# Kernel tuning notes

Hardware: AMD Instinct MI355X
Metric: run time of the kernel (lower is better)

The kernel has to match this reference:

```python
import jax, jax.numpy as jnp
import numpy as np

NOPE, ROPE, VDIM, QKD = 128, 64, 128, 192
H = 16
EPS = 1e-6
SCALING = QKD ** -0.5


def rms_norm(x, w):
    xf = x.astype(jnp.float32)
    var = jnp.mean(xf * xf, axis=-1, keepdims=True)
    return (w * (xf * jax.lax.rsqrt(var + EPS))).astype(x.dtype)


def rotate_half(x):
    d = x.shape[-1] // 2
    return jnp.concatenate((-x[..., d:], x[..., :d]), axis=-1)


def apply_rope(q, k, cos, sin):
    # cos/sin: [B,S,D] -> unsqueeze head dim
    cos = cos[:, None, :, :]
    sin = sin[:, None, :, :]
    return q * cos + rotate_half(q) * sin, k * cos + rotate_half(k) * sin


def setup_inputs() -> dict:
    key = jax.random.key(0)
    ks = jax.random.split(key, 8)
    B, S, D = 2, 2048, 2048
    pos = jnp.arange(S, dtype=jnp.float32)
    inv_freq = 1.0 / (10000.0 ** (jnp.arange(0, ROPE, 2, dtype=jnp.float32) / ROPE))
    ang = pos[:, None] * inv_freq[None, :]            # [S, ROPE/2]
    emb = jnp.concatenate([ang, ang], axis=-1)        # [S, ROPE]
    cos = jnp.broadcast_to(jnp.cos(emb)[None], (B, S, ROPE))
    sin = jnp.broadcast_to(jnp.sin(emb)[None], (B, S, ROPE))
    s = lambda k, shp, fan: jax.random.normal(k, shp, jnp.float32) * (fan ** -0.5)
    return {
        "hidden_states": jax.random.normal(ks[0], (B, S, D), jnp.float32),
        "cos": cos,
        "sin": sin,
        "q_a_W": s(ks[1], (1536, D), D),
        "q_a_norm_w": jnp.ones((1536,), jnp.float32),
        "q_b_W": s(ks[2], (H * QKD, 1536), 1536),
        "kv_a_W": s(ks[3], (512 + ROPE, D), D),
        "kv_a_norm_w": jnp.ones((512,), jnp.float32),
        "kv_b_W": s(ks[4], (H * (NOPE + VDIM), 512), 512),
        "o_W": s(ks[5], (D, H * VDIM), H * VDIM),
    }


def reference(hidden_states, cos, sin, q_a_W, q_a_norm_w, q_b_W, kv_a_W,
              kv_a_norm_w, kv_b_W, o_W):
    B, S, D = hidden_states.shape
    # low-rank Q path
    q = rms_norm(hidden_states @ q_a_W.T, q_a_norm_w) @ q_b_W.T   # [B,S,H*QKD]
    q = q.reshape(B, S, H, QKD).transpose(0, 2, 1, 3)             # [B,H,S,QKD]
    q_pass, q_rot = q[..., :NOPE], q[..., NOPE:]
    # compressed KV path
    ckv = hidden_states @ kv_a_W.T                                # [B,S,512+ROPE]
    k_lat, k_rot = ckv[..., :512], ckv[..., 512:]
    kv = rms_norm(k_lat, kv_a_norm_w) @ kv_b_W.T                  # [B,S,H*(NOPE+VDIM)]
    kv = kv.reshape(B, S, H, NOPE + VDIM).transpose(0, 2, 1, 3)   # [B,H,S,*]
    k_pass, v = kv[..., :NOPE], kv[..., NOPE:]
    k_rot = k_rot.reshape(B, 1, S, ROPE)
    q_rot, k_rot = apply_rope(q_rot, k_rot, cos, sin)
    k_rot = jnp.broadcast_to(k_rot, (B, H, S, ROPE))
    query = jnp.concatenate((q_pass, q_rot), axis=-1)             # [B,H,S,QKD]
    key = jnp.concatenate((k_pass, k_rot), axis=-1)
    # eager causal attention
    scores = jnp.einsum('bhsd,bhtd->bhst', query, key) * SCALING
    causal = jnp.tril(jnp.ones((S, S), bool))
    scores = jnp.where(causal, scores, jnp.finfo(scores.dtype).min)
    attn = jax.nn.softmax(scores.astype(jnp.float32), axis=-1).astype(query.dtype)
    out = jnp.einsum('bhst,bhtd->bhsd', attn, v)                  # [B,H,S,VDIM]
    out = out.transpose(0, 2, 1, 3).reshape(B, S, H * VDIM)
    return out @ o_W.T
```

## Files before the change

### kernel.cpp

```cpp
#include <hip/hip_runtime.h>
#include <hip/hip_bf16.h>


typedef __bf16 bf16x8 __attribute__((ext_vector_type(8)));
typedef float floatx4 __attribute__((ext_vector_type(4)));
#define BF16 __hip_bfloat16

static __device__ __forceinline__ BF16 f2b(float x) { return __float2bfloat16(x); }
static __device__ __forceinline__ unsigned short b2u(BF16 x) { return *(unsigned short*)&x; }
static __device__ __forceinline__ float fast_exp2(float x) { return __builtin_amdgcn_exp2f(x); }

template<int CTRL>
static __device__ __forceinline__ float dpp_mov(float x) {
  int xi = __builtin_bit_cast(int, x);
  int yi = __builtin_amdgcn_update_dpp(xi, xi, CTRL, 0xF, 0xF, false);
  return __builtin_bit_cast(float, yi);
}
static __device__ __forceinline__ float row_allmax(float x) {
  x = fmaxf(x, dpp_mov<0xB1>(x));
  x = fmaxf(x, dpp_mov<0x4E>(x));
  x = fmaxf(x, dpp_mov<0x141>(x));
  x = fmaxf(x, dpp_mov<0x140>(x));
  return x;
}
static __device__ __forceinline__ float row_allsum(float x) {
  x += dpp_mov<0xB1>(x);
  x += dpp_mov<0x4E>(x);
  x += dpp_mov<0x141>(x);
  x += dpp_mov<0x140>(x);
  return x;
}

static __device__ __forceinline__ void load_lds16(const BF16* g, BF16* l) {
  __builtin_amdgcn_global_load_lds((__attribute__((address_space(1))) void*)(void*)g,
                                   (__attribute__((address_space(3))) void*)(void*)l,
                                   16, 0, 0);
}

struct CastArgs {
  const float* src[6];
  BF16* dst[6];
  long n[6];
};
__global__ void cast_multi_k(CastArgs a) {
  int r = blockIdx.y;
  long n = a.n[r];
  const float* __restrict__ x = a.src[r];
  BF16* __restrict__ y = a.dst[r];
  for (long i = ((long)blockIdx.x * 256 + threadIdx.x) * 4; i + 3 < n;
       i += (long)gridDim.x * 1024) {
    float4 v = *(const float4*)(x + i);
    y[i+0] = f2b(v.x); y[i+1] = f2b(v.y); y[i+2] = f2b(v.z); y[i+3] = f2b(v.w);
  }
}

template<int OUT_MODE>
static __device__ __forceinline__ void gemm_body(
    const BF16* __restrict__ A, const BF16* __restrict__ B, void* __restrict__ C,
    int M, int N, int K, const float* __restrict__ cosb, const float* __restrict__ sinb,
    BF16* __restrict__ P1, BF16* __restrict__ P2, int bx, int by, BF16* As, BF16* Bs) {
  int tid = threadIdx.x, wave = tid >> 6, lane = tid & 63;
  int wr = wave >> 1, wc = wave & 1, lr = lane & 15, quad = lane >> 4;
  long m0 = (long)by * 256, n0 = (long)bx * 128;

  long asrc[4]; int adst[4];
#pragma unroll
  for (int i = 0; i < 4; i++) {
    int c = wave*64 + lane + 512*i;
    int r = c >> 3, k = c & 7;
    asrc[i] = (m0 + r) * (long)K + ((k ^ (r & 7)) << 3);
    adst[i] = wave*512 + i*4096;
  }
  long bsrc[2]; int bdst[2];
#pragma unroll
  for (int i = 0; i < 2; i++) {
    int c = wave*64 + lane + 512*i;
    int r = c >> 3, k = c & 7;
    long bn = n0 + r; if (bn >= N) bn = N - 1;
    bsrc[i] = bn * (long)K + ((k ^ (r & 7)) << 3);
    bdst[i] = wave*512 + i*4096;
  }

  auto stage = [&](int bi, int kt) {
    long k0 = (long)kt << 6;
    BF16* Ad = As + bi*16384;
    BF16* Bd = Bs + bi*8192;
#pragma unroll
    for (int i = 0; i < 4; i++) load_lds16(A + asrc[i] + k0, Ad + adst[i]);
#pragma unroll
    for (int i = 0; i < 2; i++) load_lds16(B + bsrc[i] + k0, Bd + bdst[i]);
  };

  int aoff[4], boff[4];
#pragma unroll
  for (int i = 0; i < 4; i++) aoff[i] = (wr*64 + i*16 + lr) * 64;
#pragma unroll
  for (int j = 0; j < 4; j++) boff[j] = (wc*64 + j*16 + lr) * 64;
  int x0 = ((quad    ) ^ (lr & 7)) << 3;
  int x1 = ((quad ^ 4) ^ (lr & 7)) << 3;

  floatx4 acc[4][4] = {};
  int NT = K >> 6;

  stage(0, 0);
  stage(1, 1);
  asm volatile("s_waitcnt vmcnt(6)" ::: "memory");
  __builtin_amdgcn_s_barrier();

  int cur = 0;
  for (int t = 0; t < NT; t++) {
    const BF16* Ab = As + cur*16384;
    const BF16* Bb = Bs + cur*8192;
    bf16x8 a0[4], a1[4], b0[4], b1[4];
#pragma unroll
    for (int i = 0; i < 4; i++) {
      a0[i] = *(const bf16x8*)(Ab + aoff[i] + x0);
      a1[i] = *(const bf16x8*)(Ab + aoff[i] + x1);
    }
#pragma unroll
    for (int j = 0; j < 4; j++) {
      b0[j] = *(const bf16x8*)(Bb + boff[j] + x0);
      b1[j] = *(const bf16x8*)(Bb + boff[j] + x1);
    }
    asm volatile("s_waitcnt lgkmcnt(0)" ::: "memory");
    __builtin_amdgcn_s_barrier();
    if (t + 2 < NT) stage(cur, t + 2);
    __builtin_amdgcn_s_setprio(1);
#pragma unroll
    for (int i = 0; i < 4; i++)
#pragma unroll
      for (int j = 0; j < 4; j++)
        acc[i][j] = __builtin_amdgcn_mfma_f32_16x16x32_bf16(a0[i], b0[j], acc[i][j], 0, 0, 0);
#pragma unroll
    for (int i = 0; i < 4; i++)
#pragma unroll
      for (int j = 0; j < 4; j++)
        acc[i][j] = __builtin_amdgcn_mfma_f32_16x16x32_bf16(a1[i], b1[j], acc[i][j], 0, 0, 0);
    __builtin_amdgcn_s_setprio(0);
    if (t + 2 < NT)      { asm volatile("s_waitcnt vmcnt(6)" ::: "memory"); }
    else if (t + 1 < NT) { asm volatile("s_waitcnt vmcnt(0)" ::: "memory"); }
    __builtin_amdgcn_s_barrier();
    __builtin_amdgcn_sched_barrier(0);
    cur ^= 1;
  }

  long n0w = n0 + wc*64;
  const float SCALE_L2E = 0.104117546f;
#pragma unroll
  for (int i = 0; i < 4; i++) {
    long tok = m0 + wr*64 + i*16 + quad*4;
    long bb = tok >> 11, s = tok & 2047;
    if (OUT_MODE == 0) {
#pragma unroll
      for (int r = 0; r < 4; r++) {
        long row = tok + r;
#pragma unroll
        for (int j = 0; j < 4; j++) {
          long col = n0w + j*16 + lr;
          if (col < N) ((float*)C)[row*(long)N + col] = acc[i][j][r];
        }
      }
    } else if (OUT_MODE == 2) {
#pragma unroll
      for (int j = 0; j < 4; j++) {
        long col = n0w + j*16 + lr;
        long h = col >> 8, d = col & 255;
        if (d < 128) {
#pragma unroll
          for (int r = 0; r < 4; r++)
            P1[((bb*16 + h)*2048 + s + r)*192 + d] = f2b(acc[i][j][r]);
        } else {
          ushort4 pk;
          pk.x = b2u(f2b(acc[i][j][0])); pk.y = b2u(f2b(acc[i][j][1]));
          pk.z = b2u(f2b(acc[i][j][2])); pk.w = b2u(f2b(acc[i][j][3]));
          *(ushort4*)(P2 + ((bb*16 + h)*128 + d - 128)*2048 + s) = pk;
        }
      }
    } else {
      bool rope = ((n0w % 192) == 128);
#pragma unroll
      for (int r = 0; r < 4; r++) {
        long row = tok + r;
#pragma unroll
        for (int j = 0; j < 4; j++) {
          long col = n0w + j*16 + lr;
          float x = acc[i][j][r], val;
          if (rope) {
            int id = j*16 + lr;
            float partner = acc[i][j^2][r];
            float rot = (j < 2) ? -partner : partner;
            val = x*cosb[row*64 + id] + rot*sinb[row*64 + id];
          } else {
            val = x;
          }
          long h = col / 192, d = col % 192;
          P1[((bb*16 + h)*2048 + s + r)*192 + d] = f2b(val * SCALE_L2E);
        }
      }
    }
  }
}

__global__ __launch_bounds__(512) void gemm0_k(const BF16* __restrict__ A, const BF16* __restrict__ B,
                                               float* __restrict__ C, int M, int N, int K) {
  __shared__ __align__(16) BF16 As[2*256*64];
  __shared__ __align__(16) BF16 Bs[2*128*64];
  gemm_body<0>(A, B, C, M, N, K, nullptr, nullptr, nullptr, nullptr,
               blockIdx.x, blockIdx.y, As, Bs);
}

__global__ __launch_bounds__(512) void gemm_qkv_k(const BF16* __restrict__ qan, const BF16* __restrict__ Wqb,
                                                  const BF16* __restrict__ kvn, const BF16* __restrict__ Wkvb,
                                                  const float* __restrict__ cosb, const float* __restrict__ sinb,
                                                  BF16* __restrict__ Qt, BF16* __restrict__ Kt,
                                                  BF16* __restrict__ Vt) {
  __shared__ __align__(16) BF16 As[2*256*64];
  __shared__ __align__(16) BF16 Bs[2*128*64];
  int bid = blockIdx.x;
  if (bid < 384) {
    gemm_body<3>(qan, Wqb, nullptr, 4096, 3072, 1536, cosb, sinb, Qt, nullptr,
                 bid % 24, bid / 24, As, Bs);
  } else {
    bid -= 384;
    gemm_body<2>(kvn, Wkvb, nullptr, 4096, 4096, 512, nullptr, nullptr, Kt, Vt,
                 bid % 32, bid / 32, As, Bs);
  }
}

__global__ __launch_bounds__(256) void norms_k(const float* __restrict__ qakv,
                                               const float* __restrict__ qw, const float* __restrict__ kw,
                                               const float* __restrict__ cosb, const float* __restrict__ sinb,
                                               BF16* __restrict__ qan, BF16* __restrict__ kvn,
                                               BF16* __restrict__ Kt) {
  long row = blockIdx.x;
  const float* xr = qakv + row * 2112;
  int tid = threadIdx.x;
  __shared__ float red[4];
  {
    float ss = 0.f;
    for (int i = tid*4; i < 1536; i += 1024) {
      float4 v = *(const float4*)(xr + i);
      ss += v.x*v.x + v.y*v.y + v.z*v.z + v.w*v.w;
    }
#pragma unroll
    for (int off = 32; off > 0; off >>= 1) ss += __shfl_down(ss, off);
    if ((tid & 63) == 0) red[tid >> 6] = ss;
    __syncthreads();
    float rs = rsqrtf((red[0]+red[1]+red[2]+red[3]) / 1536.f + 1e-6f);
    BF16* yr = qan + row * 1536;
    for (int i = tid*4; i < 1536; i += 1024) {
      float4 v = *(const float4*)(xr + i);
      yr[i+0] = f2b(v.x * qw[i+0] * rs);
      yr[i+1] = f2b(v.y * qw[i+1] * rs);
      yr[i+2] = f2b(v.z * qw[i+2] * rs);
      yr[i+3] = f2b(v.w * qw[i+3] * rs);
    }
  }
  __syncthreads();
  {
    float ss = 0.f;
    for (int i = tid*4; i < 512; i += 1024) {
      float4 v = *(const float4*)(xr + 1536 + i);
      ss += v.x*v.x + v.y*v.y + v.z*v.z + v.w*v.w;
    }
#pragma unroll
    for (int off = 32; off > 0; off >>= 1) ss += __shfl_down(ss, off);
    if ((tid & 63) == 0) red[tid >> 6] = ss;
    __syncthreads();
    float rs = rsqrtf((red[0]+red[1]+red[2]+red[3]) / 512.f + 1e-6f);
    BF16* yr = kvn + row * 512;
    for (int i = tid*4; i < 512; i += 1024) {
      float4 v = *(const float4*)(xr + 1536 + i);
      yr[i+0] = f2b(v.x * kw[i+0] * rs);
      yr[i+1] = f2b(v.y * kw[i+1] * rs);
      yr[i+2] = f2b(v.z * kw[i+2] * rs);
      yr[i+3] = f2b(v.w * kw[i+3] * rs);
    }
  }
  if (tid < 64) {
    int i = tid;
    const float* kr = xr + 2048;
    float x = kr[i];
    float rot = (i < 32) ? -kr[i + 32] : kr[i - 32];
    BF16 v = f2b(x * cosb[row*64 + i] + rot * sinb[row*64 + i]);
    long b = row >> 11, s = row & 2047;
    long base = ((b*16)*2048 + s)*192 + 128 + i;
#pragma unroll
    for (int h = 0; h < 16; h++) Kt[base + (long)h*2048*192] = v;
  }
}

#define LK 200
#define LV 72
#define LP 72
__global__ __launch_bounds__(512) void flash_k(const BF16* __restrict__ Qt, const BF16* __restrict__ Kt,
                                               const BF16* __restrict__ Vt, BF16* __restrict__ O) {
  __shared__ __align__(16) BF16 Ks[64*LK];
  __shared__ __align__(16) BF16 Vs[128*LV];
  __shared__ __align__(16) BF16 Ps[8][16*LP];
  int tid = threadIdx.x, wave = tid >> 6, lane = tid & 63;
  int lr = lane & 15, quad = lane >> 4;
  int F = blockIdx.x;
  int g = F & 31, u = F >> 5;
  int qt = (u < 8) ? u : 23 - u;
  int h = g & 15, b = g >> 4;
  const BF16* Qb = Qt + ((long)(b*16 + h) * 2048) * 192;
  const BF16* Kb = Kt + ((long)(b*16 + h) * 2048) * 192;
  const BF16* Vb = Vt + ((long)(b*16 + h) * 128) * 2048;
  const float NEG_INF = -__builtin_inff();

  int krow[3], kcol[3];
#pragma unroll
  for (int i = 0; i < 3; i++) {
    int c = tid + 512*i;
    krow[i] = c / 24; kcol[i] = (c % 24) * 8;
  }
  int vrow[2], vcol[2];
#pragma unroll
  for (int i = 0; i < 2; i++) {
    int c = tid + 512*i;
    vrow[i] = c >> 3; vcol[i] = (c & 7) * 8;
  }

  bf16x8 kreg[3], vreg[2];
  auto stage_load = [&](int k0) {
#pragma unroll
    for (int i = 0; i < 3; i++)
      kreg[i] = *(const bf16x8*)(Kb + (long)(k0 + krow[i])*192 + kcol[i]);
#pragma unroll
    for (int i = 0; i < 2; i++)
      vreg[i] = *(const bf16x8*)(Vb + (long)vrow[i]*2048 + k0 + vcol[i]);
  };
  auto stage_store = [&]() {
#pragma unroll
    for (int i = 0; i < 3; i++)
      *(bf16x8*)(Ks + krow[i]*LK + kcol[i]) = kreg[i];
#pragma unroll
    for (int i = 0; i < 2; i++)
      *(bf16x8*)(Vs + vrow[i]*LV + vcol[i]) = vreg[i];
  };

  {
    int q0 = qt * 128;
    int wq0 = q0 + wave*16;
    bf16x8 qf[6];
    {
      const BF16* qp = Qb + (long)(wq0 + lr) * 192 + quad*8;
#pragma unroll
      for (int f = 0; f < 6; f++) qf[f] = *(const bf16x8*)(qp + f*32);
    }
    float m_i[4], l_i[4];
#pragma unroll
    for (int r = 0; r < 4; r++) { m_i[r] = NEG_INF; l_i[r] = 0.f; }
    floatx4 o_acc[8] = {};
    int nk = 2*qt + 2;
    stage_load(0);
    for (int kt = 0; kt < nk; kt++) {
      __syncthreads();
      stage_store();
      __syncthreads();
      if (kt + 1 < nk) stage_load((kt + 1) * 64);
      if (kt*64 > wq0 + 15) continue;
      floatx4 st[4];
      __builtin_amdgcn_s_setprio(1);
#pragma unroll
      for (int t = 0; t < 4; t++) {
        floatx4 c = {};
#pragma unroll
        for (int f = 0; f < 6; f++) {
          bf16x8 kf = *(const bf16x8*)(Ks + (t*16+lr)*LK + f*32 + quad*8);
          c = __builtin_amdgcn_mfma_f32_16x16x32_bf16(qf[f], kf, c, 0, 0, 0);
        }
        st[t] = c;
      }
      __builtin_amdgcn_s_setprio(0);
      float mt[4];
#pragma unroll
      for (int r = 0; r < 4; r++) mt[r] = NEG_INF;
      if (kt*64 + 63 > wq0) {
        int rbase = wq0 + quad*4 - kt*64;
#pragma unroll
        for (int t = 0; t < 4; t++) {
          int coff = t*16 + lr;
#pragma unroll
          for (int r = 0; r < 4; r++) {
            float sc = st[t][r];
            if (coff > rbase + r) sc = NEG_INF;
            st[t][r] = sc;
            mt[r] = fmaxf(mt[r], sc);
          }
        }
      } else {
#pragma unroll
        for (int t = 0; t < 4; t++)
#pragma unroll
          for (int r = 0; r < 4; r++) mt[r] = fmaxf(mt[r], st[t][r]);
      }
#pragma unroll
      for (int r = 0; r < 4; r++) mt[r] = row_allmax(mt[r]);
      float alpha[4], rsum[4];
#pragma unroll
      for (int r = 0; r < 4; r++) {
        float mn = fmaxf(m_i[r], mt[r]);
        alpha[r] = fast_exp2(m_i[r] - mn);
        m_i[r] = mn;
        rsum[r] = 0.f;
      }
#pragma unroll
      for (int t = 0; t < 4; t++)
#pragma unroll
        for (int r = 0; r < 4; r++) {
          float p = fast_exp2(st[t][r] - m_i[r]);
          st[t][r] = p;
          rsum[r] += p;
        }
#pragma unroll
      for (int r = 0; r < 4; r++) rsum[r] = row_allsum(rsum[r]);
#pragma unroll
      for (int r = 0; r < 4; r++) l_i[r] = l_i[r]*alpha[r] + rsum[r];
#pragma unroll
      for (int v = 0; v < 8; v++)
#pragma unroll
        for (int r = 0; r < 4; r++) o_acc[v][r] *= alpha[r];
#pragma unroll
      for (int t = 0; t < 4; t++)
#pragma unroll
        for (int r = 0; r < 4; r++)
          Ps[wave][(quad*4 + r)*LP + t*16 + lr] = f2b(st[t][r]);
      __builtin_amdgcn_s_setprio(1);
#pragma unroll
      for (int kc = 0; kc < 2; kc++) {
        bf16x8 pa = *(const bf16x8*)(&Ps[wave][lr*LP + kc*32 + quad*8]);
#pragma unroll
        for (int v = 0; v < 8; v++) {
          bf16x8 vf = *(const bf16x8*)(&Vs[(v*16+lr)*LV + kc*32 + quad*8]);
          o_acc[v] = __builtin_amdgcn_mfma_f32_16x16x32_bf16(pa, vf, o_acc[v], 0, 0, 0);
        }
      }
      __builtin_amdgcn_s_setprio(0);
    }
    long rowb = wq0 + quad*4;
#pragma unroll
    for (int v = 0; v < 8; v++)
#pragma unroll
      for (int r = 0; r < 4; r++) {
        long row = rowb + r;
        O[((long)b*2048 + row)*2048 + h*128 + v*16 + lr] = f2b(o_acc[v][r] / l_i[r]);
      }
  }
}

extern "C" void kernel_launch(void* const* d_in, const int* in_sizes, int n_in,
                              void* d_out, int out_size, void* d_ws, size_t ws_size,
                              hipStream_t stream) {
  const float* hidden      = (const float*)d_in[0];
  const float* cosb        = (const float*)d_in[1];
  const float* sinb        = (const float*)d_in[2];
  const float* q_a_W       = (const float*)d_in[3];
  const float* q_a_norm_w  = (const float*)d_in[4];
  const float* q_b_W       = (const float*)d_in[5];
  const float* kv_a_W      = (const float*)d_in[6];
  const float* kv_a_norm_w = (const float*)d_in[7];
  const float* kv_b_W      = (const float*)d_in[8];
  const float* o_W         = (const float*)d_in[9];
  float* out = (float*)d_out;

  const int Mrows = 4096;

  char* ws = (char*)d_ws; size_t off = 0;
  auto alloc = [&](size_t bytes) -> void* {
    void* p = ws + off; off = (off + bytes + 255) & ~(size_t)255; return p;
  };
  BF16* hb    = (BF16*)alloc((size_t)4096*2048*2);
  BF16* Wqakv = (BF16*)alloc((size_t)2112*2048*2);
  BF16* Wqb   = (BF16*)alloc((size_t)3072*1536*2);
  BF16* Wkvb  = (BF16*)alloc((size_t)4096*512*2);
  BF16* Wo    = (BF16*)alloc((size_t)2048*2048*2);
  float* qakv = (float*)alloc((size_t)4096*2112*4);
  BF16* qan   = (BF16*)alloc((size_t)4096*1536*2);
  BF16* kvn   = (BF16*)alloc((size_t)4096*512*2);
  BF16* Qt    = (BF16*)alloc((size_t)2*16*2048*192*2);
  BF16* Kt    = (BF16*)alloc((size_t)2*16*2048*192*2);
  BF16* Vt    = (BF16*)alloc((size_t)2*16*128*2048*2);
  BF16* attn  = (BF16*)alloc((size_t)4096*2048*2);

  CastArgs ca;
  ca.src[0] = hidden;  ca.dst[0] = hb;                 ca.n[0] = (long)4096*2048;
  ca.src[1] = q_a_W;   ca.dst[1] = Wqakv;              ca.n[1] = (long)1536*2048;
  ca.src[2] = kv_a_W;  ca.dst[2] = Wqakv + (long)1536*2048; ca.n[2] = (long)576*2048;
  ca.src[3] = q_b_W;   ca.dst[3] = Wqb;                ca.n[3] = (long)3072*1536;
  ca.src[4] = kv_b_W;  ca.dst[4] = Wkvb;               ca.n[4] = (long)4096*512;
  ca.src[5] = o_W;     ca.dst[5] = Wo;                 ca.n[5] = (long)2048*2048;
  cast_multi_k<<<dim3(1024, 6), dim3(256), 0, stream>>>(ca);

  gemm0_k<<<dim3(17, 16), dim3(512), 0, stream>>>(hb, Wqakv, qakv, Mrows, 2112, 2048);

  norms_k<<<dim3(4096), dim3(256), 0, stream>>>(qakv, q_a_norm_w, kv_a_norm_w,
                                                cosb, sinb, qan, kvn, Kt);

  gemm_qkv_k<<<dim3(896), dim3(512), 0, stream>>>(qan, Wqb, kvn, Wkvb, cosb, sinb, Qt, Kt, Vt);

  flash_k<<<dim3(512), dim3(512), 0, stream>>>(Qt, Kt, Vt, attn);

  gemm0_k<<<dim3(16, 16), dim3(512), 0, stream>>>(attn, Wo, out, Mrows, 2048, 2048);
}
```

Baseline: 446.3 us.

## Double-buffer K/V tiles in flash attention and add lazy softmax rescaling

K and V shared-memory tiles are double-buffered so the next tile is written into the alternate buffer after compute. This removes one of the two block-wide barriers per iteration and overlaps global loads with compute. Online-softmax rescaling of the accumulator and running sum is now skipped unless the running max grows by more than a threshold anywhere in the wave, which saves exp and multiply work. In exchange, shared memory per block nearly doubles, which may lower occupancy, and unscaled exponentials can grow larger between rescales.

```diff
diff --git a/kernel.cpp b/kernel.cpp
--- a/kernel.cpp
+++ b/kernel.cpp
@@ -295,8 +295,8 @@
 #define LP 72
 __global__ __launch_bounds__(512) void flash_k(const BF16* __restrict__ Qt, const BF16* __restrict__ Kt,
                                                const BF16* __restrict__ Vt, BF16* __restrict__ O) {
-  __shared__ __align__(16) BF16 Ks[64*LK];
-  __shared__ __align__(16) BF16 Vs[128*LV];
+  __shared__ __align__(16) BF16 Ks[2][64*LK];
+  __shared__ __align__(16) BF16 Vs[2][128*LV];
   __shared__ __align__(16) BF16 Ps[8][16*LP];
   int tid = threadIdx.x, wave = tid >> 6, lane = tid & 63;
   int lr = lane & 15, quad = lane >> 4;
@@ -331,13 +331,13 @@
     for (int i = 0; i < 2; i++)
       vreg[i] = *(const bf16x8*)(Vb + (long)vrow[i]*2048 + k0 + vcol[i]);
   };
-  auto stage_store = [&]() {
+  auto stage_store = [&](int s) {
 #pragma unroll
     for (int i = 0; i < 3; i++)
-      *(bf16x8*)(Ks + krow[i]*LK + kcol[i]) = kreg[i];
+      *(bf16x8*)(&Ks[s][krow[i]*LK + kcol[i]]) = kreg[i];
 #pragma unroll
     for (int i = 0; i < 2; i++)
-      *(bf16x8*)(Vs + vrow[i]*LV + vcol[i]) = vreg[i];
+      *(bf16x8*)(&Vs[s][vrow[i]*LV + vcol[i]]) = vreg[i];
   };
 
   {
@@ -355,89 +355,99 @@
     floatx4 o_acc[8] = {};
     int nk = 2*qt + 2;
     stage_load(0);
+    stage_store(0);
+    __syncthreads();
+    int cur = 0;
     for (int kt = 0; kt < nk; kt++) {
+      if (kt + 1 < nk) stage_load((kt + 1) * 64);
+      if (kt*64 <= wq0 + 15) {
+        const BF16* Kc = Ks[cur];
+        const BF16* Vc = Vs[cur];
+        floatx4 st[4];
+        __builtin_amdgcn_s_setprio(1);
+#pragma unroll
+        for (int t = 0; t < 4; t++) {
+          floatx4 c = {};
+#pragma unroll
+          for (int f = 0; f < 6; f++) {
+            bf16x8 kf = *(const bf16x8*)(Kc + (t*16+lr)*LK + f*32 + quad*8);
+            c = __builtin_amdgcn_mfma_f32_16x16x32_bf16(qf[f], kf, c, 0, 0, 0);
+          }
+          st[t] = c;
+        }
+        __builtin_amdgcn_s_setprio(0);
+        float mt[4];
+#pragma unroll
+        for (int r = 0; r < 4; r++) mt[r] = NEG_INF;
+        if (kt*64 + 63 > wq0) {
+          int rbase = wq0 + quad*4 - kt*64;
+#pragma unroll
+          for (int t = 0; t < 4; t++) {
+            int coff = t*16 + lr;
+#pragma unroll
+            for (int r = 0; r < 4; r++) {
+              float sc = st[t][r];
+              if (coff > rbase + r) sc = NEG_INF;
+              st[t][r] = sc;
+              mt[r] = fmaxf(mt[r], sc);
+            }
+          }
+        } else {
+#pragma unroll
+          for (int t = 0; t < 4; t++)
+#pragma unroll
+            for (int r = 0; r < 4; r++) mt[r] = fmaxf(mt[r], st[t][r]);
+        }
+#pragma unroll
+        for (int r = 0; r < 4; r++) mt[r] = row_allmax(mt[r]);
+        float gr = fmaxf(fmaxf(mt[0]-m_i[0], mt[1]-m_i[1]),
+                         fmaxf(mt[2]-m_i[2], mt[3]-m_i[3]));
+        gr = fmaxf(gr, __shfl_xor(gr, 16));
+        gr = fmaxf(gr, __shfl_xor(gr, 32));
+        if (gr > 8.f) {
+#pragma unroll
+          for (int r = 0; r < 4; r++) {
+            float mn = fmaxf(m_i[r], mt[r]);
+            float alpha = fast_exp2(m_i[r] - mn);
+            m_i[r] = mn;
+            l_i[r] *= alpha;
+#pragma unroll
+            for (int v = 0; v < 8; v++) o_acc[v][r] *= alpha;
+          }
+        }
+        float rsum[4];
+#pragma unroll
+        for (int r = 0; r < 4; r++) rsum[r] = 0.f;
+#pragma unroll
+        for (int t = 0; t < 4; t++)
+#pragma unroll
+          for (int r = 0; r < 4; r++) {
+            float p = fast_exp2(st[t][r] - m_i[r]);
+            st[t][r] = p;
+            rsum[r] += p;
+          }
+#pragma unroll
+        for (int r = 0; r < 4; r++) { rsum[r] = row_allsum(rsum[r]); l_i[r] += rsum[r]; }
+#pragma unroll
+        for (int t = 0; t < 4; t++)
+#pragma unroll
+          for (int r = 0; r < 4; r++)
+            Ps[wave][(quad*4 + r)*LP + t*16 + lr] = f2b(st[t][r]);
+        __builtin_amdgcn_s_setprio(1);
+#pragma unroll
+        for (int kc = 0; kc < 2; kc++) {
+          bf16x8 pa = *(const bf16x8*)(&Ps[wave][lr*LP + kc*32 + quad*8]);
+#pragma unroll
+          for (int v = 0; v < 8; v++) {
+            bf16x8 vf = *(const bf16x8*)(&Vc[(v*16+lr)*LV + kc*32 + quad*8]);
+            o_acc[v] = __builtin_amdgcn_mfma_f32_16x16x32_bf16(pa, vf, o_acc[v], 0, 0, 0);
+          }
+        }
+        __builtin_amdgcn_s_setprio(0);
+      }
+      if (kt + 1 < nk) stage_store(cur ^ 1);
       __syncthreads();
-      stage_store();
-      __syncthreads();
-      if (kt + 1 < nk) stage_load((kt + 1) * 64);
-      if (kt*64 > wq0 + 15) continue;
-      floatx4 st[4];
-      __builtin_amdgcn_s_setprio(1);
-#pragma unroll
-      for (int t = 0; t < 4; t++) {
-        floatx4 c = {};
-#pragma unroll
-        for (int f = 0; f < 6; f++) {
-          bf16x8 kf = *(const bf16x8*)(Ks + (t*16+lr)*LK + f*32 + quad*8);
-          c = __builtin_amdgcn_mfma_f32_16x16x32_bf16(qf[f], kf, c, 0, 0, 0);
-        }
-        st[t] = c;
-      }
-      __builtin_amdgcn_s_setprio(0);
-      float mt[4];
-#pragma unroll
-      for (int r = 0; r < 4; r++) mt[r] = NEG_INF;
-      if (kt*64 + 63 > wq0) {
-        int rbase = wq0 + quad*4 - kt*64;
-#pragma unroll
-        for (int t = 0; t < 4; t++) {
-          int coff = t*16 + lr;
-#pragma unroll
-          for (int r = 0; r < 4; r++) {
-            float sc = st[t][r];
-            if (coff > rbase + r) sc = NEG_INF;
-            st[t][r] = sc;
-            mt[r] = fmaxf(mt[r], sc);
-          }
-        }
-      } else {
-#pragma unroll
-        for (int t = 0; t < 4; t++)
-#pragma unroll
-          for (int r = 0; r < 4; r++) mt[r] = fmaxf(mt[r], st[t][r]);
-      }
-#pragma unroll
-      for (int r = 0; r < 4; r++) mt[r] = row_allmax(mt[r]);
-      float alpha[4], rsum[4];
-#pragma unroll
-      for (int r = 0; r < 4; r++) {
-        float mn = fmaxf(m_i[r], mt[r]);
-        alpha[r] = fast_exp2(m_i[r] - mn);
-        m_i[r] = mn;
-        rsum[r] = 0.f;
-      }
-#pragma unroll
-      for (int t = 0; t < 4; t++)
-#pragma unroll
-        for (int r = 0; r < 4; r++) {
-          float p = fast_exp2(st[t][r] - m_i[r]);
-          st[t][r] = p;
-          rsum[r] += p;
-        }
-#pragma unroll
-      for (int r = 0; r < 4; r++) rsum[r] = row_allsum(rsum[r]);
-#pragma unroll
-      for (int r = 0; r < 4; r++) l_i[r] = l_i[r]*alpha[r] + rsum[r];
-#pragma unroll
-      for (int v = 0; v < 8; v++)
-#pragma unroll
-        for (int r = 0; r < 4; r++) o_acc[v][r] *= alpha[r];
-#pragma unroll
-      for (int t = 0; t < 4; t++)
-#pragma unroll
-        for (int r = 0; r < 4; r++)
-          Ps[wave][(quad*4 + r)*LP + t*16 + lr] = f2b(st[t][r]);
-      __builtin_amdgcn_s_setprio(1);
-#pragma unroll
-      for (int kc = 0; kc < 2; kc++) {
-        bf16x8 pa = *(const bf16x8*)(&Ps[wave][lr*LP + kc*32 + quad*8]);
-#pragma unroll
-        for (int v = 0; v < 8; v++) {
-          bf16x8 vf = *(const bf16x8*)(&Vs[(v*16+lr)*LV + kc*32 + quad*8]);
-          o_acc[v] = __builtin_amdgcn_mfma_f32_16x16x32_bf16(pa, vf, o_acc[v], 0, 0, 0);
-        }
-      }
-      __builtin_amdgcn_s_setprio(0);
+      cur ^= 1;
     }
     long rowb = wq0 + quad*4;
 #pragma unroll
```

Result: no change. 450.1 us (+0.9%).

## Split LDS fragment loads to overlap MFMA and add XCD-aware block swizzle

Applied to the files above, without the earlier changes.

The GEMM inner loop now issues the first half of the LDS fragment reads, starts the first MFMA batch while the second half is still in flight, and only then waits and synchronises. The aim is to hide LDS read latency behind matrix math. Block indices in the GEMM kernels are also remapped so that consecutive tiles land on the same XCD, which should improve L2 reuse across the chiplets. The swizzle assumes the workgroup count divides evenly by 8, and the explicit waitcnt and sched_barrier placement is fragile.

```diff
diff --git a/kernel.cpp b/kernel.cpp
--- a/kernel.cpp
+++ b/kernel.cpp
@@ -35,6 +35,11 @@
   __builtin_amdgcn_global_load_lds((__attribute__((address_space(1))) void*)(void*)g,
                                    (__attribute__((address_space(3))) void*)(void*)l,
                                    16, 0, 0);
+}
+
+static __device__ __forceinline__ int xcd_swz(int bid, int nwg) {
+  int cpx = nwg >> 3;
+  return (bid & 7) * cpx + (bid >> 3);
 }
 
 struct CastArgs {
@@ -113,24 +118,27 @@
     const BF16* Bb = Bs + cur*8192;
     bf16x8 a0[4], a1[4], b0[4], b1[4];
 #pragma unroll
-    for (int i = 0; i < 4; i++) {
-      a0[i] = *(const bf16x8*)(Ab + aoff[i] + x0);
-      a1[i] = *(const bf16x8*)(Ab + aoff[i] + x1);
-    }
-#pragma unroll
-    for (int j = 0; j < 4; j++) {
-      b0[j] = *(const bf16x8*)(Bb + boff[j] + x0);
-      b1[j] = *(const bf16x8*)(Bb + boff[j] + x1);
-    }
+    for (int i = 0; i < 4; i++) a0[i] = *(const bf16x8*)(Ab + aoff[i] + x0);
+#pragma unroll
+    for (int j = 0; j < 4; j++) b0[j] = *(const bf16x8*)(Bb + boff[j] + x0);
+    __builtin_amdgcn_sched_barrier(0);
+#pragma unroll
+    for (int i = 0; i < 4; i++) a1[i] = *(const bf16x8*)(Ab + aoff[i] + x1);
+#pragma unroll
+    for (int j = 0; j < 4; j++) b1[j] = *(const bf16x8*)(Bb + boff[j] + x1);
+    asm volatile("s_waitcnt lgkmcnt(8)" ::: "memory");
+    __builtin_amdgcn_sched_barrier(0);
+    __builtin_amdgcn_s_setprio(1);
+#pragma unroll
+    for (int i = 0; i < 4; i++)
+#pragma unroll
+      for (int j = 0; j < 4; j++)
+        acc[i][j] = __builtin_amdgcn_mfma_f32_16x16x32_bf16(a0[i], b0[j], acc[i][j], 0, 0, 0);
+    __builtin_amdgcn_s_setprio(0);
     asm volatile("s_waitcnt lgkmcnt(0)" ::: "memory");
     __builtin_amdgcn_s_barrier();
     if (t + 2 < NT) stage(cur, t + 2);
     __builtin_amdgcn_s_setprio(1);
-#pragma unroll
-    for (int i = 0; i < 4; i++)
-#pragma unroll
-      for (int j = 0; j < 4; j++)
-        acc[i][j] = __builtin_amdgcn_mfma_f32_16x16x32_bf16(a0[i], b0[j], acc[i][j], 0, 0, 0);
 #pragma unroll
     for (int i = 0; i < 4; i++)
 #pragma unroll
@@ -205,8 +213,11 @@
                                                float* __restrict__ C, int M, int N, int K) {
   __shared__ __align__(16) BF16 As[2*256*64];
   __shared__ __align__(16) BF16 Bs[2*128*64];
+  int nwg = gridDim.x * gridDim.y;
+  int lin = blockIdx.y * gridDim.x + blockIdx.x;
+  int s = xcd_swz(lin, nwg);
   gemm_body<0>(A, B, C, M, N, K, nullptr, nullptr, nullptr, nullptr,
-               blockIdx.x, blockIdx.y, As, Bs);
+               s % gridDim.x, s / gridDim.x, As, Bs);
 }
 
 __global__ __launch_bounds__(512) void gemm_qkv_k(const BF16* __restrict__ qan, const BF16* __restrict__ Wqb,
@@ -218,12 +229,14 @@
   __shared__ __align__(16) BF16 Bs[2*128*64];
   int bid = blockIdx.x;
   if (bid < 384) {
+    int s = xcd_swz(bid, 384);
     gemm_body<3>(qan, Wqb, nullptr, 4096, 3072, 1536, cosb, sinb, Qt, nullptr,
-                 bid % 24, bid / 24, As, Bs);
+                 s % 24, s / 24, As, Bs);
   } else {
     bid -= 384;
+    int s = xcd_swz(bid, 512);
     gemm_body<2>(kvn, Wkvb, nullptr, 4096, 4096, 512, nullptr, nullptr, Kt, Vt,
-                 bid % 32, bid / 32, As, Bs);
+                 s % 32, s / 32, As, Bs);
   }
 }
 
```

Result: no change. 449.3 us (+0.7%).
